# Kernel optimization log

Hardware: AMD Instinct MI355X
Metric: run time of the kernel (lower is better)

The kernel has to match this reference:

```python
import jax, jax.numpy as jnp
import numpy as np

S = 8192      # s: number of persons/nodes
F = 1024      # feature_len
A = 256       # attn_len
SIGMA_X, SIGMA_Y = 4.0, 1.0
EPS_VALID = 1e-8
EPS_DIS = 1e-4


def setup_inputs() -> dict:
    key = jax.random.key(0)
    ks = jax.random.split(key, 8)
    batch_data = jax.random.normal(ks[0], (S, F), dtype=jnp.float32)
    xywh = jax.random.uniform(ks[1], (S, 4), dtype=jnp.float32)  # positive -> all rows valid
    actor_weights = jax.random.uniform(ks[2], (S,), dtype=jnp.float32)
    avg_pos = jax.random.uniform(ks[3], (S, 2), dtype=jnp.float32)
    # learned params (kaiming-ish init, zero bias as in original)
    W_h = jax.random.normal(ks[4], (F, 2), dtype=jnp.float32) * (2.0 / F) ** 0.5
    b_h = jnp.zeros((2,), dtype=jnp.float32)
    W_g = jax.random.normal(ks[5], (F, A), dtype=jnp.float32) * (2.0 / F) ** 0.5
    b_g = jnp.zeros((A,), dtype=jnp.float32)
    return {
        "batch_data": batch_data, "xywh": xywh, "OW": 1920, "OH": 1080,
        "actor_weights": actor_weights, "avg_pos": avg_pos,
        "W_h": W_h, "b_h": b_h, "W_g": W_g, "b_g": b_g, "num_person": S,
    }


def reference(batch_data, xywh, OW, OH, actor_weights, avg_pos, W_h, b_h, W_g, b_g, num_person):
    # highlight_fc + tanh -> predicted offsets [S,2]
    hp = jnp.tanh(batch_data @ W_h + b_h)
    hx = hp[:, 0] * xywh[:, 2] * SIGMA_X + xywh[:, 0]  # [S]
    hy = hp[:, 1] * xywh[:, 3] * SIGMA_Y + xywh[:, 1]  # [S]

    # gcn_fc + relu -> node messages [S,A]
    targets = jax.nn.relu(batch_data @ W_g + b_g)

    # valid rows/cols: torch loop skips i/j with sum(xywh) < 1e-8
    valid = jnp.sum(xywh, axis=1) >= EPS_VALID  # [S] bool

    # pairwise inverse-distance weights [S,S] (the memory-bound core)
    dx = hx[:, None] - xywh[None, :, 0]
    dy = hy[:, None] - xywh[None, :, 1]
    dis = jnp.sqrt(dx * dx + dy * dy)
    pair_valid = valid[:, None] & valid[None, :]
    w = jnp.where(pair_valid, 1.0 / (dis + EPS_DIS), 0.0)
    row_sum = jnp.sum(w, axis=1, keepdims=True)
    w = jnp.where(valid[:, None], w / jnp.maximum(row_sum, 1e-30), 0.0)

    targets_weighted = w @ targets  # [S,A]
    return (targets_weighted, hp)
```

## Files before the change

kernel.cpp:

```cpp
#include <hip/hip_runtime.h>
#include <math.h>
#include <stdint.h>

typedef __attribute__((ext_vector_type(8))) short short8;
typedef __attribute__((ext_vector_type(4))) float f32x4;

__device__ __forceinline__ uint32_t cvt_pk_bf16(float lo, float hi) {
  uint32_t r;
  asm("v_cvt_pk_bf16_f32 %0, %1, %2" : "=v"(r) : "v"(lo), "v"(hi));
  return r;
}

__device__ __forceinline__ float wfun(float hx, float hy, float cx, float cy) {
  float dx = hx - cx, dy = hy - cy;
  float d = __builtin_amdgcn_sqrtf(fmaf(dx, dx, dy * dy));
  return __builtin_amdgcn_rcpf(d + 1e-4f);
}

__global__ __launch_bounds__(256) void k_prep_w(
    const float* __restrict__ Wg, uint16_t* __restrict__ WgT, int F, int A) {
  int idx = blockIdx.x * 256 + threadIdx.x;
  int a = idx % A;
  int k0 = (idx / A) * 8;
  if (k0 >= F) return;
  float f[8];
  #pragma unroll
  for (int e = 0; e < 8; ++e) f[e] = Wg[(size_t)(k0 + e) * A + a];
  uint4 v;
  v.x = cvt_pk_bf16(f[0], f[1]);
  v.y = cvt_pk_bf16(f[2], f[3]);
  v.z = cvt_pk_bf16(f[4], f[5]);
  v.w = cvt_pk_bf16(f[6], f[7]);
  *(uint4*)(WgT + (size_t)a * F + k0) = v;
}

__global__ __launch_bounds__(256) void k_fused_tgt_head(
    const float* __restrict__ batch, const uint16_t* __restrict__ WgT,
    const float* __restrict__ bg, const float* __restrict__ W_h,
    const float* __restrict__ b_h, const float* __restrict__ xywh,
    uint16_t* __restrict__ tgt2, float* __restrict__ hp_out,
    float* __restrict__ hx, float* __restrict__ hy,
    float* __restrict__ validf, float2* __restrict__ cxy,
    int S, int F, int A) {
  int t = threadIdx.x;
  int lane = t & 63, wid = t >> 6;
  int wm = wid >> 1, wn = wid & 1;
  int i0 = blockIdx.x * 32;
  int row = i0 + wm * 16 + (lane & 15);
  int kch = lane >> 4;
  const float* ab = batch + (size_t)row * F + kch * 8;
  int ncol0 = wn * 128 + (lane & 15);
  const uint16_t* bb = WgT + (size_t)ncol0 * F + kch * 8;

  f32x4 acc[8] = {};
  float wh0 = 0.f, wh1 = 0.f;
  float4 a0 = *(const float4*)(ab);
  float4 a1 = *(const float4*)(ab + 4);
  short8 bf[8];
  #pragma unroll
  for (int nf = 0; nf < 8; ++nf)
    bf[nf] = *(const short8*)(bb + (size_t)nf * 16 * F);

  for (int k0 = 0; k0 < F; k0 += 32) {
    int kn = (k0 + 32 < F) ? k0 + 32 : 0;
    float4 na0 = *(const float4*)(ab + kn);
    float4 na1 = *(const float4*)(ab + kn + 4);
    short8 nbf[8];
    #pragma unroll
    for (int nf = 0; nf < 8; ++nf)
      nbf[nf] = *(const short8*)(bb + kn + (size_t)nf * 16 * F);

    if (wn == 0) {
      const float* whp = W_h + 2 * (k0 + kch * 8);
      float4 h0 = *(const float4*)(whp);
      float4 h1 = *(const float4*)(whp + 4);
      float4 h2 = *(const float4*)(whp + 8);
      float4 h3 = *(const float4*)(whp + 12);
      wh0 += a0.x*h0.x + a0.y*h0.z + a0.z*h1.x + a0.w*h1.z
           + a1.x*h2.x + a1.y*h2.z + a1.z*h3.x + a1.w*h3.z;
      wh1 += a0.x*h0.y + a0.y*h0.w + a0.z*h1.y + a0.w*h1.w
           + a1.x*h2.y + a1.y*h2.w + a1.z*h3.y + a1.w*h3.w;
    }

    union { short8 s; uint32_t u[4]; } af;
    af.u[0] = cvt_pk_bf16(a0.x, a0.y);
    af.u[1] = cvt_pk_bf16(a0.z, a0.w);
    af.u[2] = cvt_pk_bf16(a1.x, a1.y);
    af.u[3] = cvt_pk_bf16(a1.z, a1.w);
    #pragma unroll
    for (int nf = 0; nf < 8; ++nf)
      acc[nf] = __builtin_amdgcn_mfma_f32_16x16x32_bf16(af.s, bf[nf], acc[nf], 0, 0, 0);
    a0 = na0; a1 = na1;
    #pragma unroll
    for (int nf = 0; nf < 8; ++nf) bf[nf] = nbf[nf];
  }

  int jb = blockIdx.x;
  int rloc = wm * 16 + (lane >> 4) * 4;
  #pragma unroll
  for (int nf = 0; nf < 8; ++nf) {
    int col = ncol0 + nf * 16;
    float b = bg[col];
    float o0 = fmaxf(acc[nf][0] + b, 0.f);
    float o1 = fmaxf(acc[nf][1] + b, 0.f);
    float o2 = fmaxf(acc[nf][2] + b, 0.f);
    float o3 = fmaxf(acc[nf][3] + b, 0.f);
    uint2 pk;
    pk.x = cvt_pk_bf16(o0, o1);
    pk.y = cvt_pk_bf16(o2, o3);
    *(uint2*)(tgt2 + ((size_t)jb * A + col) * 32 + rloc) = pk;
  }

  if (wn == 0) {
    wh0 += __shfl_xor(wh0, 16, 64);
    wh0 += __shfl_xor(wh0, 32, 64);
    wh1 += __shfl_xor(wh1, 16, 64);
    wh1 += __shfl_xor(wh1, 32, 64);
    if (lane < 16) {
      int r = i0 + wm * 16 + lane;
      float hp0 = tanhf(wh0 + b_h[0]);
      float hp1 = tanhf(wh1 + b_h[1]);
      float4 xy = ((const float4*)xywh)[r];
      hp_out[2 * r] = hp0;
      hp_out[2 * r + 1] = hp1;
      hx[r] = hp0 * xy.z * 4.0f + xy.x;
      hy[r] = hp1 * xy.w * 1.0f + xy.y;
      bool v = (xy.x + xy.y + xy.z + xy.w >= 1e-8f);
      validf[r] = v ? 1.0f : 0.0f;
      cxy[r] = v ? make_float2(xy.x, xy.y) : make_float2(1e30f, 1e30f);
    }
  }
}

__global__ __launch_bounds__(1024, 4) void k_gather_v20(
    const uint16_t* __restrict__ tgt2, const float2* __restrict__ cxy,
    const float* __restrict__ hx, const float* __restrict__ hy,
    const float* __restrict__ validf, float* __restrict__ out, int S, int A) {
  __shared__ uint16_t Bt[2][4][128][40];
  __shared__ uint32_t Af[2][4][2][2][64][4];
  __shared__ float comb[64][132];
  __shared__ float rs_l[4][64][4];
  __shared__ float scale_s[64];

  int t = threadIdx.x;
  int lane = t & 63, wid = t >> 6;
  int kg = wid >> 2;
  int sub = wid & 3;
  int wm = sub >> 1, wn = sub & 1;
  int colhalf = blockIdx.x;
  int i0 = blockIdx.y * 64;
  int kch = lane >> 4;
  int n0 = wn * 64 + (lane & 15);
  int NT = S / (4 * 32);
  const size_t TSTRIDE = (size_t)A * 32;
  const int COLS = 40;

  int wkg = t >> 8;
  int v = t & 255;
  int wr = v & 63;
  int z = v >> 6;
  int m2 = (z & 1) * 2;
  int h0 = z >> 1;
  float hx_w = hx[i0 + wr], hy_w = hy[i0 + wr];
  int rgw = wr >> 5, wmw = (wr >> 4) & 1, rl = wr & 15;
  uint32_t* afA0 = &Af[0][wkg][wmw][rgw][rl | (h0 << 4)][m2];
  uint32_t* afB0 = &Af[0][wkg][wmw][rgw][rl | ((h0 + 2) << 4)][m2];
  uint32_t* afA1 = &Af[1][wkg][wmw][rgw][rl | (h0 << 4)][m2];
  uint32_t* afB1 = &Af[1][wkg][wmw][rgw][rl | ((h0 + 2) << 4)][m2];
  const float2* gC = cxy + (size_t)wkg * (S >> 2);
  int cOffA = 8 * h0 + 2 * m2;
  int cOffB = cOffA + 16;

  int scol = v >> 1;
  int skw = v & 1;
  const uint16_t* gB0 = tgt2 + (size_t)(wkg * NT) * TSTRIDE
                        + (size_t)(colhalf * 128 + scol) * 32 + skw * 16;

  f32x4 acc0[4] = {};
  f32x4 acc1[4] = {};
  float rs = 0.f;

  {
    uint4 ga = *(const uint4*)(gB0);
    uint4 gb = *(const uint4*)(gB0 + 8);
    *(uint4*)&Bt[0][wkg][scol][skw * 16] = ga;
    *(uint4*)&Bt[0][wkg][scol][skw * 16 + 8] = gb;
    float4 ca = *(const float4*)(gC + cOffA);
    float4 cb = *(const float4*)(gC + cOffA + 2);
    float4 cc = *(const float4*)(gC + cOffB);
    float4 cd = *(const float4*)(gC + cOffB + 2);
    float w0 = wfun(hx_w, hy_w, ca.x, ca.y);
    float w1 = wfun(hx_w, hy_w, ca.z, ca.w);
    float w2 = wfun(hx_w, hy_w, cb.x, cb.y);
    float w3 = wfun(hx_w, hy_w, cb.z, cb.w);
    float w4 = wfun(hx_w, hy_w, cc.x, cc.y);
    float w5 = wfun(hx_w, hy_w, cc.z, cc.w);
    float w6 = wfun(hx_w, hy_w, cd.x, cd.y);
    float w7 = wfun(hx_w, hy_w, cd.z, cd.w);
    rs += ((w0 + w1) + (w2 + w3)) + ((w4 + w5) + (w6 + w7));
    uint2 pA = make_uint2(cvt_pk_bf16(w0, w1), cvt_pk_bf16(w2, w3));
    uint2 pB = make_uint2(cvt_pk_bf16(w4, w5), cvt_pk_bf16(w6, w7));
    *(uint2*)afA0 = pA;
    *(uint2*)afB0 = pB;
  }
  __syncthreads();

  for (int ts = 0; ts < NT; ++ts) {
    int cur = ts & 1, nxt = cur ^ 1;
    int tn = (ts + 1 < NT) ? ts + 1 : 0;

    const uint16_t* bp = gB0 + (size_t)tn * TSTRIDE;
    uint4 ga = *(const uint4*)(bp);
    uint4 gb = *(const uint4*)(bp + 8);
    const float2* cp = gC + (size_t)tn * 32;
    float4 ca = *(const float4*)(cp + cOffA);
    float4 cb = *(const float4*)(cp + cOffA + 2);
    float4 cc = *(const float4*)(cp + cOffB);
    float4 cd = *(const float4*)(cp + cOffB + 2);

    short8 a0 = *(const short8*)&Af[cur][kg][wm][0][lane][0];
    short8 a1 = *(const short8*)&Af[cur][kg][wm][1][lane][0];
    const uint16_t* br = &Bt[cur][kg][n0][kch * 8];
    short8 b0 = *(const short8*)(br);
    short8 b1 = *(const short8*)(br + 16 * COLS);
    short8 b2 = *(const short8*)(br + 32 * COLS);
    short8 b3 = *(const short8*)(br + 48 * COLS);

    acc0[0] = __builtin_amdgcn_mfma_f32_16x16x32_bf16(a0, b0, acc0[0], 0, 0, 0);
    acc0[1] = __builtin_amdgcn_mfma_f32_16x16x32_bf16(a0, b1, acc0[1], 0, 0, 0);
    acc0[2] = __builtin_amdgcn_mfma_f32_16x16x32_bf16(a0, b2, acc0[2], 0, 0, 0);
    acc0[3] = __builtin_amdgcn_mfma_f32_16x16x32_bf16(a0, b3, acc0[3], 0, 0, 0);
    acc1[0] = __builtin_amdgcn_mfma_f32_16x16x32_bf16(a1, b0, acc1[0], 0, 0, 0);
    acc1[1] = __builtin_amdgcn_mfma_f32_16x16x32_bf16(a1, b1, acc1[1], 0, 0, 0);
    acc1[2] = __builtin_amdgcn_mfma_f32_16x16x32_bf16(a1, b2, acc1[2], 0, 0, 0);
    acc1[3] = __builtin_amdgcn_mfma_f32_16x16x32_bf16(a1, b3, acc1[3], 0, 0, 0);

    float w0 = wfun(hx_w, hy_w, ca.x, ca.y);
    float w1 = wfun(hx_w, hy_w, ca.z, ca.w);
    float w2 = wfun(hx_w, hy_w, cb.x, cb.y);
    float w3 = wfun(hx_w, hy_w, cb.z, cb.w);
    float w4 = wfun(hx_w, hy_w, cc.x, cc.y);
    float w5 = wfun(hx_w, hy_w, cc.z, cc.w);
    float w6 = wfun(hx_w, hy_w, cd.x, cd.y);
    float w7 = wfun(hx_w, hy_w, cd.z, cd.w);
    float g = (ts + 1 < NT) ? 1.f : 0.f;
    rs = fmaf(g, ((w0 + w1) + (w2 + w3)) + ((w4 + w5) + (w6 + w7)), rs);
    uint2 pA = make_uint2(cvt_pk_bf16(w0, w1), cvt_pk_bf16(w2, w3));
    uint2 pB = make_uint2(cvt_pk_bf16(w4, w5), cvt_pk_bf16(w6, w7));
    *(uint2*)(nxt ? afA1 : afA0) = pA;
    *(uint2*)(nxt ? afB1 : afB0) = pB;

    *(uint4*)&Bt[nxt][wkg][scol][skw * 16] = ga;
    *(uint4*)&Bt[nxt][wkg][scol][skw * 16 + 8] = gb;
    __syncthreads();
  }

  rs_l[wkg][wr][z] = rs;
  int rbase = (lane >> 4) * 4;

  if (kg == 1) {
    #pragma unroll
    for (int r = 0; r < 4; ++r) {
      int r0 = wm * 16 + rbase + r, r1 = 32 + r0;
      comb[r0][n0]      = acc0[0][r];
      comb[r0][n0 + 16] = acc0[1][r];
      comb[r0][n0 + 32] = acc0[2][r];
      comb[r0][n0 + 48] = acc0[3][r];
      comb[r1][n0]      = acc1[0][r];
      comb[r1][n0 + 16] = acc1[1][r];
      comb[r1][n0 + 32] = acc1[2][r];
      comb[r1][n0 + 48] = acc1[3][r];
    }
  }
  __syncthreads();
  if (t < 64) {
    float r = 0.f;
    #pragma unroll
    for (int k2 = 0; k2 < 4; ++k2)
      #pragma unroll
      for (int z2 = 0; z2 < 4; ++z2) r += rs_l[k2][t][z2];
    float fv = validf[i0 + t];
    scale_s[t] = (fv > 0.f) ? 1.0f / fmaxf(r, 1e-30f) : 0.f;
  }
  if (kg == 0) {
    #pragma unroll
    for (int r = 0; r < 4; ++r) {
      int r0 = wm * 16 + rbase + r, r1 = 32 + r0;
      acc0[0][r] += comb[r0][n0];
      acc0[1][r] += comb[r0][n0 + 16];
      acc0[2][r] += comb[r0][n0 + 32];
      acc0[3][r] += comb[r0][n0 + 48];
      acc1[0][r] += comb[r1][n0];
      acc1[1][r] += comb[r1][n0 + 16];
      acc1[2][r] += comb[r1][n0 + 32];
      acc1[3][r] += comb[r1][n0 + 48];
    }
  }
  __syncthreads();
  if (kg == 2) {
    #pragma unroll
    for (int r = 0; r < 4; ++r) {
      int r0 = wm * 16 + rbase + r, r1 = 32 + r0;
      comb[r0][n0]      = acc0[0][r];
      comb[r0][n0 + 16] = acc0[1][r];
      comb[r0][n0 + 32] = acc0[2][r];
      comb[r0][n0 + 48] = acc0[3][r];
      comb[r1][n0]      = acc1[0][r];
      comb[r1][n0 + 16] = acc1[1][r];
      comb[r1][n0 + 32] = acc1[2][r];
      comb[r1][n0 + 48] = acc1[3][r];
    }
  }
  __syncthreads();
  if (kg == 0) {
    #pragma unroll
    for (int r = 0; r < 4; ++r) {
      int r0 = wm * 16 + rbase + r, r1 = 32 + r0;
      acc0[0][r] += comb[r0][n0];
      acc0[1][r] += comb[r0][n0 + 16];
      acc0[2][r] += comb[r0][n0 + 32];
      acc0[3][r] += comb[r0][n0 + 48];
      acc1[0][r] += comb[r1][n0];
      acc1[1][r] += comb[r1][n0 + 16];
      acc1[2][r] += comb[r1][n0 + 32];
      acc1[3][r] += comb[r1][n0 + 48];
    }
  }
  __syncthreads();
  if (kg == 3) {
    #pragma unroll
    for (int r = 0; r < 4; ++r) {
      int r0 = wm * 16 + rbase + r, r1 = 32 + r0;
      comb[r0][n0]      = acc0[0][r];
      comb[r0][n0 + 16] = acc0[1][r];
      comb[r0][n0 + 32] = acc0[2][r];
      comb[r0][n0 + 48] = acc0[3][r];
      comb[r1][n0]      = acc1[0][r];
      comb[r1][n0 + 16] = acc1[1][r];
      comb[r1][n0 + 32] = acc1[2][r];
      comb[r1][n0 + 48] = acc1[3][r];
    }
  }
  __syncthreads();
  if (kg == 0) {
    int cb = colhalf * 128;
    #pragma unroll
    for (int r = 0; r < 4; ++r) {
      int r0 = wm * 16 + rbase + r, r1 = 32 + r0;
      float s0 = scale_s[r0], s1 = scale_s[r1];
      size_t b0o = (size_t)(i0 + r0) * A + cb;
      size_t b1o = (size_t)(i0 + r1) * A + cb;
      out[b0o + n0]      = (acc0[0][r] + comb[r0][n0]) * s0;
      out[b0o + n0 + 16] = (acc0[1][r] + comb[r0][n0 + 16]) * s0;
      out[b0o + n0 + 32] = (acc0[2][r] + comb[r0][n0 + 32]) * s0;
      out[b0o + n0 + 48] = (acc0[3][r] + comb[r0][n0 + 48]) * s0;
      out[b1o + n0]      = (acc1[0][r] + comb[r1][n0]) * s1;
      out[b1o + n0 + 16] = (acc1[1][r] + comb[r1][n0 + 16]) * s1;
      out[b1o + n0 + 32] = (acc1[2][r] + comb[r1][n0 + 32]) * s1;
      out[b1o + n0 + 48] = (acc1[3][r] + comb[r1][n0 + 48]) * s1;
    }
  }
}

extern "C" void kernel_launch(void* const* d_in, const int* in_sizes, int n_in,
                              void* d_out, int out_size, void* d_ws, size_t ws_size,
                              hipStream_t stream) {
  const float* batch = (const float*)d_in[0];
  const float* xywh  = (const float*)d_in[1];
  const float* W_h   = (const float*)d_in[6];
  const float* b_h   = (const float*)d_in[7];
  const float* W_g   = (const float*)d_in[8];
  const float* b_g   = (const float*)d_in[9];
  int S = in_sizes[4];
  int F = in_sizes[0] / S;
  int A = in_sizes[9];

  float* out    = (float*)d_out;
  float* out_tw = out;
  float* out_hp = out + (size_t)S * A;

  uint16_t* tgt2 = (uint16_t*)d_ws;
  uint16_t* WgT  = tgt2 + (size_t)A * S;
  float* hxv = (float*)(WgT + (size_t)A * F);
  float* hyv = hxv + S;
  float* vfv = hyv + S;
  float2* cxyv = (float2*)(vfv + S);

  k_prep_w<<<dim3((A * F / 8 + 255) / 256), 256, 0, stream>>>(W_g, WgT, F, A);
  k_fused_tgt_head<<<dim3(S / 32), 256, 0, stream>>>(batch, WgT, b_g, W_h, b_h,
                                                     xywh, tgt2, out_hp, hxv,
                                                     hyv, vfv, cxyv, S, F, A);
  k_gather_v20<<<dim3(2, S / 64), 1024, 0, stream>>>(tgt2, cxyv, hxv, hyv, vfv,
                                                     out_tw, S, A);
}
```

Baseline: 131.9 us.

## Split K dimension across two warp groups in fused target/head GEMM

The fused target/head kernel now runs 512 threads per block, with two groups of four waves each handling half of the K (feature) dimension. The second group writes its partial accumulators and head dot-products to shared memory. After a block barrier the first group adds them in before applying bias/ReLU and tanh. This aims to raise parallelism and latency hiding in a GEMM whose grid has only S/32 blocks, at the cost of about 33KB of shared memory and an extra sync.

```diff
diff --git a/kernel.cpp b/kernel.cpp
--- a/kernel.cpp
+++ b/kernel.cpp
@@ -34,7 +34,7 @@
   *(uint4*)(WgT + (size_t)a * F + k0) = v;
 }
 
-__global__ __launch_bounds__(256) void k_fused_tgt_head(
+__global__ __launch_bounds__(512) void k_fused_tgt_head(
     const float* __restrict__ batch, const uint16_t* __restrict__ WgT,
     const float* __restrict__ bg, const float* __restrict__ W_h,
     const float* __restrict__ b_h, const float* __restrict__ xywh,
@@ -42,15 +42,23 @@
     float* __restrict__ hx, float* __restrict__ hy,
     float* __restrict__ validf, float2* __restrict__ cxy,
     int S, int F, int A) {
+  __shared__ float comb[32][258];
+  __shared__ float whl0[2][16];
+  __shared__ float whl1[2][16];
+
   int t = threadIdx.x;
   int lane = t & 63, wid = t >> 6;
-  int wm = wid >> 1, wn = wid & 1;
+  int tk = wid >> 2;
+  int sub = wid & 3;
+  int wm = sub >> 1, wn = sub & 1;
   int i0 = blockIdx.x * 32;
   int row = i0 + wm * 16 + (lane & 15);
   int kch = lane >> 4;
-  const float* ab = batch + (size_t)row * F + kch * 8;
+  int KH = F >> 1;
+  int kbase = tk * KH;
+  const float* ab = batch + (size_t)row * F + kbase + kch * 8;
   int ncol0 = wn * 128 + (lane & 15);
-  const uint16_t* bb = WgT + (size_t)ncol0 * F + kch * 8;
+  const uint16_t* bb = WgT + (size_t)ncol0 * F + kbase + kch * 8;
 
   f32x4 acc[8] = {};
   float wh0 = 0.f, wh1 = 0.f;
@@ -61,8 +69,8 @@
   for (int nf = 0; nf < 8; ++nf)
     bf[nf] = *(const short8*)(bb + (size_t)nf * 16 * F);
 
-  for (int k0 = 0; k0 < F; k0 += 32) {
-    int kn = (k0 + 32 < F) ? k0 + 32 : 0;
+  for (int k0 = 0; k0 < KH; k0 += 32) {
+    int kn = (k0 + 32 < KH) ? k0 + 32 : 0;
     float4 na0 = *(const float4*)(ab + kn);
     float4 na1 = *(const float4*)(ab + kn + 4);
     short8 nbf[8];
@@ -71,7 +79,7 @@
       nbf[nf] = *(const short8*)(bb + kn + (size_t)nf * 16 * F);
 
     if (wn == 0) {
-      const float* whp = W_h + 2 * (k0 + kch * 8);
+      const float* whp = W_h + 2 * (kbase + k0 + kch * 8);
       float4 h0 = *(const float4*)(whp);
       float4 h1 = *(const float4*)(whp + 4);
       float4 h2 = *(const float4*)(whp + 8);
@@ -95,31 +103,49 @@
     for (int nf = 0; nf < 8; ++nf) bf[nf] = nbf[nf];
   }
 
-  int jb = blockIdx.x;
-  int rloc = wm * 16 + (lane >> 4) * 4;
-  #pragma unroll
-  for (int nf = 0; nf < 8; ++nf) {
-    int col = ncol0 + nf * 16;
-    float b = bg[col];
-    float o0 = fmaxf(acc[nf][0] + b, 0.f);
-    float o1 = fmaxf(acc[nf][1] + b, 0.f);
-    float o2 = fmaxf(acc[nf][2] + b, 0.f);
-    float o3 = fmaxf(acc[nf][3] + b, 0.f);
-    uint2 pk;
-    pk.x = cvt_pk_bf16(o0, o1);
-    pk.y = cvt_pk_bf16(o2, o3);
-    *(uint2*)(tgt2 + ((size_t)jb * A + col) * 32 + rloc) = pk;
-  }
-
+  int mre = wm * 16 + (lane >> 4) * 4;
+  if (tk == 1) {
+    #pragma unroll
+    for (int nf = 0; nf < 8; ++nf) {
+      int col = ncol0 + nf * 16;
+      #pragma unroll
+      for (int r = 0; r < 4; ++r) comb[mre + r][col] = acc[nf][r];
+    }
+  }
   if (wn == 0) {
     wh0 += __shfl_xor(wh0, 16, 64);
     wh0 += __shfl_xor(wh0, 32, 64);
     wh1 += __shfl_xor(wh1, 16, 64);
     wh1 += __shfl_xor(wh1, 32, 64);
-    if (lane < 16) {
+    if (tk == 1 && lane < 16) {
+      whl0[wm][lane] = wh0;
+      whl1[wm][lane] = wh1;
+    }
+  }
+  __syncthreads();
+
+  if (tk == 0) {
+    int jb = blockIdx.x;
+    int rloc = mre;
+    #pragma unroll
+    for (int nf = 0; nf < 8; ++nf) {
+      int col = ncol0 + nf * 16;
+      float b = bg[col];
+      float o0 = fmaxf(acc[nf][0] + comb[rloc][col] + b, 0.f);
+      float o1 = fmaxf(acc[nf][1] + comb[rloc + 1][col] + b, 0.f);
+      float o2 = fmaxf(acc[nf][2] + comb[rloc + 2][col] + b, 0.f);
+      float o3 = fmaxf(acc[nf][3] + comb[rloc + 3][col] + b, 0.f);
+      uint2 pk;
+      pk.x = cvt_pk_bf16(o0, o1);
+      pk.y = cvt_pk_bf16(o2, o3);
+      *(uint2*)(tgt2 + ((size_t)jb * A + col) * 32 + rloc) = pk;
+    }
+    if (wn == 0 && lane < 16) {
       int r = i0 + wm * 16 + lane;
-      float hp0 = tanhf(wh0 + b_h[0]);
-      float hp1 = tanhf(wh1 + b_h[1]);
+      float W0 = wh0 + whl0[wm][lane];
+      float W1 = wh1 + whl1[wm][lane];
+      float hp0 = tanhf(W0 + b_h[0]);
+      float hp1 = tanhf(W1 + b_h[1]);
       float4 xy = ((const float4*)xywh)[r];
       hp_out[2 * r] = hp0;
       hp_out[2 * r + 1] = hp1;
@@ -387,7 +413,7 @@
   float2* cxyv = (float2*)(vfv + S);
 
   k_prep_w<<<dim3((A * F / 8 + 255) / 256), 256, 0, stream>>>(W_g, WgT, F, A);
-  k_fused_tgt_head<<<dim3(S / 32), 256, 0, stream>>>(batch, WgT, b_g, W_h, b_h,
+  k_fused_tgt_head<<<dim3(S / 32), 512, 0, stream>>>(batch, WgT, b_g, W_h, b_h,
                                                      xywh, tgt2, out_hp, hxv,
                                                      hyv, vfv, cxyv, S, F, A);
   k_gather_v20<<<dim3(2, S / 64), 1024, 0, stream>>>(tgt2, cxyv, hxv, hyv, vfv,
```

Result: no change. 132.8 us (+0.7%).
